# Kernel tuning notes

Measured on AMD Instinct MI355X. Metric: run time of the kernel, lower is better.

Reference implementation:

```python
import jax, jax.numpy as jnp
import numpy as np

N, T = 128, 20
E_IN, E_EMB, E_RNN = 2, 64, 256
N_IN, N_EMB, N_RNN, N_OUT = 2, 64, 128, 5
ATT = 64

# static edge index sets: diagonal = temporal edges (i,i), off-diagonal = spatial edges (i,j)
_DIAG = np.arange(N) * N + np.arange(N)
_OFFJ = np.array([[j for j in range(N) if j != i] for i in range(N)])  # [N, N-1]
_OFFD = (np.arange(N)[:, None] * N + _OFFJ).reshape(-1)               # [N*(N-1)]
_TEMP = (N - 1) / np.sqrt(ATT)  # attention temperature = num_edges / sqrt(attention_size)


def setup_inputs() -> dict:
    ks = iter(jax.random.split(jax.random.key(0), 40))
    def p(shape, s=0.05):
        return jax.random.normal(next(ks), shape, jnp.float32) * s
    return {
        "nodes": p((T, N, N_IN), 1.0),
        "edges": p((T, N * N, E_IN), 1.0),
        "h_edge0": jnp.zeros((N * N, E_RNN), jnp.float32),
        "c_edge0": jnp.zeros((N * N, E_RNN), jnp.float32),
        "h_node0": jnp.zeros((N, N_RNN), jnp.float32),
        "c_node0": jnp.zeros((N, N_RNN), jnp.float32),
        "t_enc_w": p((E_EMB, E_IN)), "t_enc_b": p((E_EMB,)),
        "t_wih": p((4 * E_RNN, E_EMB)), "t_whh": p((4 * E_RNN, E_RNN)),
        "t_bih": p((4 * E_RNN,)), "t_bhh": p((4 * E_RNN,)),
        "s_enc_w": p((E_EMB, E_IN)), "s_enc_b": p((E_EMB,)),
        "s_wih": p((4 * E_RNN, E_EMB)), "s_whh": p((4 * E_RNN, E_RNN)),
        "s_bih": p((4 * E_RNN,)), "s_bhh": p((4 * E_RNN,)),
        "att_t_w": p((ATT, E_RNN)), "att_t_b": p((ATT,)),
        "att_s_w": p((ATT, E_RNN)), "att_s_b": p((ATT,)),
        "n_enc_w": p((N_EMB, N_IN)), "n_enc_b": p((N_EMB,)),
        "n_attn_w": p((N_EMB, 2 * E_RNN)), "n_attn_b": p((N_EMB,)),
        "n_wih": p((4 * N_RNN, 2 * N_EMB)), "n_whh": p((4 * N_RNN, N_RNN)),
        "n_bih": p((4 * N_RNN,)), "n_bhh": p((4 * N_RNN,)),
        "out_w": p((N_OUT, N_RNN)), "out_b": p((N_OUT,)),
    }


def _lstm(x, h, c, wih, whh, bih, bhh):
    g = x @ wih.T + bih + h @ whh.T + bhh
    i, f, gg, o = jnp.split(g, 4, axis=-1)
    c2 = jax.nn.sigmoid(f) * c + jax.nn.sigmoid(i) * jnp.tanh(gg)
    return jax.nn.sigmoid(o) * jnp.tanh(c2), c2


def reference(nodes, edges, h_edge0, c_edge0, h_node0, c_node0,
              t_enc_w, t_enc_b, t_wih, t_whh, t_bih, t_bhh,
              s_enc_w, s_enc_b, s_wih, s_whh, s_bih, s_bhh,
              att_t_w, att_t_b, att_s_w, att_s_b,
              n_enc_w, n_enc_b, n_attn_w, n_attn_b,
              n_wih, n_whh, n_bih, n_bhh, out_w, out_b):
    def step(carry, xt):
        h_e, c_e, h_n, c_n = carry
        pos_t, edg_t = xt
        # temporal edge RNN on self edges (i,i)
        x_t = jax.nn.relu(edg_t[_DIAG] @ t_enc_w.T + t_enc_b)
        h_t, c_t = _lstm(x_t, h_e[_DIAG], c_e[_DIAG], t_wih, t_whh, t_bih, t_bhh)
        # spatial edge RNN on all pairwise edges (i,j), i != j
        x_s = jax.nn.relu(edg_t[_OFFD] @ s_enc_w.T + s_enc_b)
        h_s, c_s = _lstm(x_s, h_e[_OFFD], c_e[_OFFD], s_wih, s_whh, s_bih, s_bhh)
        h_e = h_e.at[_DIAG].set(h_t).at[_OFFD].set(h_s)
        c_e = c_e.at[_DIAG].set(c_t).at[_OFFD].set(c_s)
        # attention: each node attends over its N-1 spatial edge hidden states
        hs = h_s.reshape(N, N - 1, E_RNN)
        te = h_t @ att_t_w.T + att_t_b                          # [N, ATT]
        se = jnp.einsum('nkd,ad->nka', hs, att_s_w) + att_s_b   # [N, N-1, ATT]
        logits = jnp.einsum('nka,na->nk', se, te) * _TEMP
        w = jax.nn.softmax(logits, axis=-1)
        weighted = jnp.einsum('nk,nkd->nd', w, hs)              # [N, E_RNN]
        # node RNN
        enc = jax.nn.relu(pos_t @ n_enc_w.T + n_enc_b)
        h_edges = jnp.concatenate([h_t, weighted], axis=-1)
        h_emb = jax.nn.relu(h_edges @ n_attn_w.T + n_attn_b)
        h_n, c_n = _lstm(jnp.concatenate([enc, h_emb], axis=-1), h_n, c_n,
                         n_wih, n_whh, n_bih, n_bhh)
        out = h_n @ out_w.T + out_b
        return (h_e, c_e, h_n, c_n), out

    _, outs = jax.lax.scan(step, (h_edge0, c_edge0, h_node0, c_node0), (nodes, edges))
    return outs  # [T, N, 5]
```

## Files before the change

kernel.cpp:

```cpp
#include <hip/hip_runtime.h>
#include <cmath>

#define NN 128
#define TT 20
#define ERNN 256
#define TEMPSC 15.875f

typedef __attribute__((ext_vector_type(8))) short bf16x8;
typedef __attribute__((ext_vector_type(4))) float f32x4;

__device__ __forceinline__ float sigm(float x){ return 1.f/(1.f+__expf(-x)); }
__device__ __forceinline__ float ftanh(float x){ float e = __expf(2.f*x); return 1.f - 2.f/(e + 1.f); }
__device__ __forceinline__ float b2f(unsigned short u){ union{unsigned int i; float f;} v; v.i = ((unsigned int)u)<<16; return v.f; }
__device__ __forceinline__ unsigned short f2b(float x){ union{float f; unsigned int u;} v; v.f = x; unsigned int r = v.u + 0x7fffu + ((v.u>>16)&1u); return (unsigned short)(r>>16); }

typedef __attribute__((address_space(3))) unsigned int lds_u32;
typedef __attribute__((address_space(1))) unsigned int glb_u32;
__device__ __forceinline__ void glds16(const void* g, void* l){
    __builtin_amdgcn_global_load_lds((const glb_u32*)g, (lds_u32*)l, 16, 0, 0);
}

__device__ __forceinline__ size_t hoff(int r, int d){
    return ((size_t)((r>>7)*32 + (d>>3))*128 + (r&127))*8 + (d&7);
}

#define R_W2    (2*1024*320)
#define R_EB    2048
#define R_NWT   131072
#define R_NBS   512
#define R_HNN   16384
#define R_CNN   16384
#define R_INIT  (16384*32)
#define R_XENC  ((size_t)TT*16384*8)
#define PREP_TOT (R_W2 + R_EB + R_NWT + R_NBS + R_HNN + R_CNN + R_INIT + R_XENC)

__global__ void k_prep_all(
    const float* __restrict__ s_wih, const float* __restrict__ s_whh, unsigned short* __restrict__ s_wHi,
    const float* __restrict__ t_wih, const float* __restrict__ t_whh, unsigned short* __restrict__ t_wHi,
    const float* __restrict__ s_bih, const float* __restrict__ s_bhh, float* __restrict__ s_bs,
    const float* __restrict__ t_bih, const float* __restrict__ t_bhh, float* __restrict__ t_bs,
    const float* __restrict__ n_wih, const float* __restrict__ n_whh, float* __restrict__ n_wT,
    const float* __restrict__ n_bih, const float* __restrict__ n_bhh, float* __restrict__ n_bs,
    const float* __restrict__ h_n0, float* __restrict__ h_nn,
    const float* __restrict__ c_n0, float* __restrict__ c_nn,
    const float* __restrict__ h_e0, const float* __restrict__ c_e0,
    unsigned short* __restrict__ hHi, unsigned short* __restrict__ c_b,
    const float* __restrict__ edges,
    const float* __restrict__ s_enc_w, const float* __restrict__ s_enc_b,
    const float* __restrict__ t_enc_w, const float* __restrict__ t_enc_b,
    unsigned short* __restrict__ xe)
{
    size_t i = (size_t)blockIdx.x*256 + threadIdx.x;
    if (i < R_W2) {
        int idx = (int)i;
        int which = idx >= 1024*320;
        if (which) idx -= 1024*320;
        const float* wih = which ? t_wih : s_wih;
        const float* whh = which ? t_whh : s_whh;
        unsigned short* wHi = which ? t_wHi : s_wHi;
        int c = idx / 320, k = idx - c*320;
        int ch = ((c>>6)<<4) + (c&15), g = (c>>4)&3;
        int r = g*256 + ch;
        float v = (k < 64) ? wih[r*64 + k] : whh[r*256 + (k-64)];
        size_t dst = ((size_t)((c>>7)*40 + (k>>3))*128 + (c&127))*8 + (k&7);
        wHi[dst] = f2b(v);
        return;
    }
    i -= R_W2;
    if (i < R_EB) {
        int c = (int)i, which = c >= 1024;
        if (which) c -= 1024;
        const float* bih = which ? t_bih : s_bih;
        const float* bhh = which ? t_bhh : s_bhh;
        float* bs = which ? t_bs : s_bs;
        int ch = ((c>>6)<<4)+(c&15), g=(c>>4)&3;
        int r = g*256+ch;
        bs[c] = bih[r] + bhh[r];
        return;
    }
    i -= R_EB;
    if (i < R_NWT) {
        int j = (int)i;
        if (j < 65536) { int r = j >> 7, c = j & 127; n_wT[c*512 + r] = n_wih[j]; }
        else { j -= 65536; int r = j >> 7, c = j & 127; n_wT[(128 + c)*512 + r] = n_whh[j]; }
        return;
    }
    i -= R_NWT;
    if (i < R_NBS) { n_bs[i] = n_bih[i] + n_bhh[i]; return; }
    i -= R_NBS;
    if (i < R_HNN) { h_nn[i] = h_n0[i]; return; }
    i -= R_HNN;
    if (i < R_CNN) { c_nn[i] = c_n0[i]; return; }
    i -= R_CNN;
    if (i < R_INIT) {
        int g = (int)i;
        int d8 = g & 31, r = g >> 5;
        int row_ij;
        if (r < 16256){ int ii = r/127, jj = r - ii*127; row_ij = ii*NN + jj + (jj>=ii ? 1:0); }
        else          { row_ij = (r - 16256)*(NN+1); }
        const float* hs = h_e0 + (size_t)row_ij*ERNN + d8*8;
        const float* cs = c_e0 + (size_t)row_ij*ERNN + d8*8;
        bf16x8 hb, cb;
        #pragma unroll
        for (int q = 0; q < 8; ++q){ hb[q] = (short)f2b(hs[q]); cb[q] = (short)f2b(cs[q]); }
        *(bf16x8*)&hHi[hoff(r, d8*8)] = hb;
        *(bf16x8*)&c_b[(size_t)r*ERNN + d8*8] = cb;
        return;
    }
    i -= R_INIT;
    if (i < R_XENC) {
        size_t g = i;
        int row = (int)(g & 127);
        size_t rest = g >> 7;
        int kc = (int)(rest & 7);
        int tile = (int)((rest >> 3) & 127);
        int t = (int)(rest >> 10);
        int r = tile*128 + row;
        bool sp = (r < 16256);
        int row_ij;
        if (sp) { int ii = r/127, jj = r - ii*127; row_ij = ii*NN + jj + (jj>=ii ? 1:0); }
        else    { row_ij = (r - 16256)*(NN+1); }
        const float* w = sp ? s_enc_w : t_enc_w;
        const float* b = sp ? s_enc_b : t_enc_b;
        float e0 = edges[((size_t)t*16384 + row_ij)*2];
        float e1 = edges[((size_t)t*16384 + row_ij)*2 + 1];
        bf16x8 v8;
        #pragma unroll
        for (int q = 0; q < 8; ++q) {
            int m = kc*8 + q;
            v8[q] = (short)f2b(fmaxf(fmaf(w[m*2], e0, fmaf(w[m*2+1], e1, b[m])), 0.f));
        }
        *(bf16x8*)&xe[g*8] = v8;
    }
}

#define ESTEP(KS, NW) do { \
    asm volatile("s_waitcnt vmcnt(" #NW ")" ::: "memory"); \
    __builtin_amdgcn_s_barrier(); \
    __builtin_amdgcn_sched_barrier(0); \
    bf16x8 a0 = *(const bf16x8*)&Ah[(KS)&1][(kg*128 + arow)*8]; \
    bf16x8 a1 = *(const bf16x8*)&Ah[(KS)&1][(kg*128 + arow + 16)*8]; \
    bf16x8 b0 = *(const bf16x8*)&Bh[(KS)&1][(kg*128 + bcol)*8]; \
    bf16x8 b1 = *(const bf16x8*)&Bh[(KS)&1][(kg*128 + bcol + 16)*8]; \
    bf16x8 b2 = *(const bf16x8*)&Bh[(KS)&1][(kg*128 + bcol + 32)*8]; \
    bf16x8 b3 = *(const bf16x8*)&Bh[(KS)&1][(kg*128 + bcol + 48)*8]; \
    asm volatile("s_waitcnt lgkmcnt(0)" ::: "memory"); \
    __builtin_amdgcn_sched_barrier(0); \
    __builtin_amdgcn_s_barrier(); \
    if ((KS) + 2 <= 9) stage((KS)+2, (KS)&1); \
    acc[0][0] = __builtin_amdgcn_mfma_f32_16x16x32_bf16(a0, b0, acc[0][0],0,0,0); \
    acc[0][1] = __builtin_amdgcn_mfma_f32_16x16x32_bf16(a0, b1, acc[0][1],0,0,0); \
    acc[0][2] = __builtin_amdgcn_mfma_f32_16x16x32_bf16(a0, b2, acc[0][2],0,0,0); \
    acc[0][3] = __builtin_amdgcn_mfma_f32_16x16x32_bf16(a0, b3, acc[0][3],0,0,0); \
    acc[1][0] = __builtin_amdgcn_mfma_f32_16x16x32_bf16(a1, b0, acc[1][0],0,0,0); \
    acc[1][1] = __builtin_amdgcn_mfma_f32_16x16x32_bf16(a1, b1, acc[1][1],0,0,0); \
    acc[1][2] = __builtin_amdgcn_mfma_f32_16x16x32_bf16(a1, b2, acc[1][2],0,0,0); \
    acc[1][3] = __builtin_amdgcn_mfma_f32_16x16x32_bf16(a1, b3, acc[1][3],0,0,0); \
} while(0)

__global__ __launch_bounds__(512) void k_fused(
    const unsigned short* __restrict__ xenc_t,
    const unsigned short* __restrict__ h_in, unsigned short* __restrict__ h_out,
    unsigned short* __restrict__ hl_out, unsigned short* __restrict__ c_b,
    const unsigned short* __restrict__ s_wHi, const float* __restrict__ s_bs,
    const unsigned short* __restrict__ t_wHi, const float* __restrict__ t_bs,
    int has_node, int n_edge,
    const float* __restrict__ nodes_prev, const unsigned short* __restrict__ hl_prev,
    float* __restrict__ h_nn, float* __restrict__ c_nn, float* __restrict__ out_prev,
    const float* __restrict__ att_t_w, const float* __restrict__ att_t_b,
    const float* __restrict__ att_s_w, const float* __restrict__ att_s_b,
    const float* __restrict__ n_enc_w, const float* __restrict__ n_enc_b,
    const float* __restrict__ n_attn_w, const float* __restrict__ n_attn_b,
    const float* __restrict__ n_wT, const float* __restrict__ n_bsum,
    const float* __restrict__ out_w, const float* __restrict__ out_b)
{
    __shared__ __align__(16) char smem[32768];
    const int bid = blockIdx.x, tid = threadIdx.x;

    if (bid < NN) {
        if (!has_node) return;
        const int i = bid;
        float* sm  = (float*)smem;
        float* ht  = sm;
        float* te  = sm + 256;
        float* u   = sm + 320;
        float* lg  = sm + 576;
        float* cat = sm + 704;
        float* xc  = sm + 1216;
        float* hnl = sm + 1344;
        float* gl  = sm + 1472;
        float* pws = sm + 1984;
        float* msc = sm + 4032;

        if (tid < 256) ht[tid] = b2f(hl_prev[(size_t)(16256 + i)*256 + tid]);
        __syncthreads();
        if (tid < 256) {
            int m = tid >> 2, q = tid & 3;
            float s = 0.f;
            const float* wr = att_t_w + m*ERNN + q*64;
            const float* hh = ht + q*64;
            #pragma unroll 8
            for (int k = 0; k < 64; ++k) s = fmaf(wr[k], hh[k], s);
            s += __shfl_xor(s, 1);
            s += __shfl_xor(s, 2);
            if (q == 0) te[m] = s + att_t_b[m];
        }
        __syncthreads();
        if (tid < 256) {
            float s = 0.f;
            for (int m = 0; m < 64; ++m) s = fmaf(att_s_w[m*ERNN + tid], te[m], s);
            u[tid] = s;
        }
        if (tid == 320) {
            float s = 0.f;
            for (int m = 0; m < 64; ++m) s = fmaf(te[m], att_s_b[m], s);
            msc[2] = s;
        }
        __syncthreads();
        {
            int slot = tid >> 2, q = tid & 3;
            float part = 0.f;
            if (slot < 127) {
                const unsigned short* hs = hl_prev + (size_t)(i*127 + slot)*256 + q*64;
                const float* uu = u + q*64;
                #pragma unroll
                for (int d8 = 0; d8 < 8; ++d8) {
                    bf16x8 v = *(const bf16x8*)(hs + d8*8);
                    #pragma unroll
                    for (int j = 0; j < 8; ++j)
                        part = fmaf(uu[d8*8 + j], b2f((unsigned short)v[j]), part);
                }
            }
            part += __shfl_xor(part, 1);
            part += __shfl_xor(part, 2);
            if (slot < 127 && q == 0) lg[slot] = (part + msc[2]) * TEMPSC;
            if (tid == 511) lg[127] = -1e30f;
        }
        __syncthreads();
        if (tid < 64) {
            float a = fmaxf(lg[tid], lg[tid+64]);
            for (int off = 32; off; off >>= 1) a = fmaxf(a, __shfl_xor(a, off));
            if (tid == 0) msc[0] = a;
        }
        __syncthreads();
        if (tid < 128) lg[tid] = (tid < 127) ? __expf(lg[tid] - msc[0]) : 0.f;
        __syncthreads();
        if (tid < 64) {
            float a = lg[tid] + lg[tid+64];
            for (int off = 32; off; off >>= 1) a += __shfl_xor(a, off);
            if (tid == 0) msc[1] = a;
        }
        __syncthreads();
        {
            int w = tid >> 6, lane = tid & 63;
            float a0 = 0.f, a1 = 0.f, a2 = 0.f, a3 = 0.f;
            #pragma unroll 4
            for (int s = w*16; s < w*16 + 16; ++s) {
                int srow = (s < 127) ? s : 0;
                float wgt = lg[s];
                const unsigned short* hs = hl_prev + (size_t)(i*127 + srow)*256 + lane*4;
                ushort4 v = *(const ushort4*)hs;
                a0 = fmaf(wgt, b2f(v.x), a0);
                a1 = fmaf(wgt, b2f(v.y), a1);
                a2 = fmaf(wgt, b2f(v.z), a2);
                a3 = fmaf(wgt, b2f(v.w), a3);
            }
            pws[w*256 + lane*4+0] = a0; pws[w*256 + lane*4+1] = a1;
            pws[w*256 + lane*4+2] = a2; pws[w*256 + lane*4+3] = a3;
        }
        if (tid >= 256 && tid < 384) hnl[tid-256] = h_nn[i*128 + (tid-256)];
        __syncthreads();
        if (tid < 256) {
            float s = 0.f;
            #pragma unroll
            for (int w = 0; w < 8; ++w) s += pws[w*256 + tid];
            cat[256 + tid] = s / msc[1];
            cat[tid] = ht[tid];
        }
        __syncthreads();
        if (tid < 64) {
            float p0 = nodes_prev[i*2], p1 = nodes_prev[i*2+1];
            xc[tid] = fmaxf(fmaf(n_enc_w[tid*2], p0, fmaf(n_enc_w[tid*2+1], p1, n_enc_b[tid])), 0.f);
        }
        if (tid >= 256) {
            int t2 = tid - 256;
            int m = t2 >> 2, q = t2 & 3;
            float s = 0.f;
            const float* wr = n_attn_w + m*512 + q*128;
            const float* cc = cat + q*128;
            #pragma unroll 8
            for (int d = 0; d < 128; ++d) s = fmaf(wr[d], cc[d], s);
            s += __shfl_xor(s, 1);
            s += __shfl_xor(s, 2);
            if (q == 0) xc[64 + m] = fmaxf(s + n_attn_b[m], 0.f);
        }
        __syncthreads();
        {
            int n = tid;
            float s = n_bsum[n];
            for (int k = 0; k < 128; ++k) s = fmaf(n_wT[k*512 + n], xc[k], s);
            for (int k = 0; k < 128; ++k) s = fmaf(n_wT[(128+k)*512 + n], hnl[k], s);
            gl[n] = s;
        }
        __syncthreads();
        if (tid < 128) {
            float co = c_nn[i*128 + tid];
            float c2 = sigm(gl[128+tid])*co + sigm(gl[tid])*ftanh(gl[256+tid]);
            float h2 = sigm(gl[384+tid])*ftanh(c2);
            c_nn[i*128+tid] = c2;
            h_nn[i*128+tid] = h2;
            hnl[tid] = h2;
        }
        __syncthreads();
        if (tid < 5) {
            float s = out_b[tid];
            const float* wr = out_w + tid*128;
            for (int k = 0; k < 128; ++k) s = fmaf(wr[k], hnl[k], s);
            out_prev[i*5 + tid] = s;
        }
        return;
    }

    if (!n_edge) return;
    unsigned short (*Ah)[4096] = (unsigned short(*)[4096])smem;
    unsigned short (*Bh)[4096] = (unsigned short(*)[4096])(smem + 16384);
    const int ebid = bid - NN;
    const int lane = tid & 63, wid = tid >> 6;
    const int wg = (ebid & 7)*128 + (ebid >> 3);
    const int bm = wg >> 3, ntp = wg & 7;
    const bool sp = (bm < 127);
    const int rbase = bm * 128;
    const unsigned short* wHi = sp ? s_wHi : t_wHi;
    const float* bs = sp ? s_bs : t_bs;
    const int wr = wid & 3, wc = wid >> 2;
    const int nt = ntp*2 + wc;

    auto stage = [&](int ks, int b){
        int kc = wid >> 1, half = wid & 1;
        const unsigned short* asrc = (ks < 2)
            ? xenc_t + ((size_t)bm*8  + ks*4     + kc)*1024 + half*512
            : h_in   + ((size_t)bm*32 + (ks-2)*4 + kc)*1024 + half*512;
        glds16(asrc + lane*8, (char*)&Ah[b][0] + wid*1024);
        size_t wb = ((size_t)(ntp*40 + ks*4 + kc)*128 + half*64)*8;
        glds16(wHi + wb + lane*8, (char*)&Bh[b][0] + wid*1024);
    };
    stage(0, 0);
    stage(1, 1);

    f32x4 acc[2][4];
    #pragma unroll
    for (int m = 0; m < 2; ++m)
        #pragma unroll
        for (int g = 0; g < 4; ++g)
            acc[m][g] = (f32x4){0.f,0.f,0.f,0.f};

    const int arow = wr*32 + (lane & 15);
    const int bcol = wc*64 + (lane & 15);
    const int kg = lane >> 4;

    ESTEP(0, 2);
    ESTEP(1, 2);
    ESTEP(2, 2);
    ESTEP(3, 2);
    ESTEP(4, 2);
    ESTEP(5, 2);
    ESTEP(6, 2);
    ESTEP(7, 2);
    ESTEP(8, 2);
    ESTEP(9, 0);

    const int chl = lane & 15, q4 = (lane >> 4)*4;
    const int ch = nt*16 + chl;
    const int cbase = nt*64 + chl;
    const float b0 = bs[cbase], b1 = bs[cbase+16], b2 = bs[cbase+32], b3 = bs[cbase+48];
    #pragma unroll
    for (int m = 0; m < 2; ++m) {
        #pragma unroll
        for (int rg = 0; rg < 4; ++rg) {
            int lrow = wr*32 + m*16 + q4 + rg;
            int row = rbase + lrow;
            float gi = acc[m][0][rg] + b0;
            float gf = acc[m][1][rg] + b1;
            float gg = acc[m][2][rg] + b2;
            float go = acc[m][3][rg] + b3;
            size_t off = (size_t)row*256 + ch;
            float c_old = b2f(c_b[off]);
            float c2 = sigm(gf)*c_old + sigm(gi)*ftanh(gg);
            float h2 = sigm(go)*ftanh(c2);
            c_b[off] = f2b(c2);
            unsigned short hb = f2b(h2);
            h_out[((size_t)(bm*32 + (ch>>3))*128 + lrow)*8 + (ch&7)] = hb;
            hl_out[off] = hb;
        }
    }
}

extern "C" void kernel_launch(void* const* d_in, const int* in_sizes, int n_in,
                              void* d_out, int out_size, void* d_ws, size_t ws_size,
                              hipStream_t stream)
{
    const float* nodes   = (const float*)d_in[0];
    const float* edges   = (const float*)d_in[1];
    const float* h_e0    = (const float*)d_in[2];
    const float* c_e0    = (const float*)d_in[3];
    const float* h_n0    = (const float*)d_in[4];
    const float* c_n0    = (const float*)d_in[5];
    const float* t_enc_w = (const float*)d_in[6];
    const float* t_enc_b = (const float*)d_in[7];
    const float* t_wih   = (const float*)d_in[8];
    const float* t_whh   = (const float*)d_in[9];
    const float* t_bih   = (const float*)d_in[10];
    const float* t_bhh   = (const float*)d_in[11];
    const float* s_enc_w = (const float*)d_in[12];
    const float* s_enc_b = (const float*)d_in[13];
    const float* s_wih   = (const float*)d_in[14];
    const float* s_whh   = (const float*)d_in[15];
    const float* s_bih   = (const float*)d_in[16];
    const float* s_bhh   = (const float*)d_in[17];
    const float* att_t_w = (const float*)d_in[18];
    const float* att_t_b = (const float*)d_in[19];
    const float* att_s_w = (const float*)d_in[20];
    const float* att_s_b = (const float*)d_in[21];
    const float* n_enc_w = (const float*)d_in[22];
    const float* n_enc_b = (const float*)d_in[23];
    const float* n_attn_w= (const float*)d_in[24];
    const float* n_attn_b= (const float*)d_in[25];
    const float* n_wih   = (const float*)d_in[26];
    const float* n_whh   = (const float*)d_in[27];
    const float* n_bih   = (const float*)d_in[28];
    const float* n_bhh   = (const float*)d_in[29];
    const float* out_w   = (const float*)d_in[30];
    const float* out_b   = (const float*)d_in[31];
    float* out = (float*)d_out;

    char* p = (char*)d_ws;
    float* h_nn  = (float*)p;            p += 128*128*4;
    float* c_nn  = (float*)p;            p += 128*128*4;
    float* s_bs  = (float*)p;            p += 1024*4;
    float* t_bs  = (float*)p;            p += 1024*4;
    float* n_wT  = (float*)p;            p += 256*512*4;
    float* n_bs  = (float*)p;            p += 512*4;
    unsigned short* c_b  = (unsigned short*)p;  p += (size_t)16384*256*2;
    unsigned short* h_a  = (unsigned short*)p;  p += (size_t)16384*256*2;
    unsigned short* h_b  = (unsigned short*)p;  p += (size_t)16384*256*2;
    unsigned short* hl_a = (unsigned short*)p;  p += (size_t)16384*256*2;
    unsigned short* hl_b = (unsigned short*)p;  p += (size_t)16384*256*2;
    unsigned short* xenc = (unsigned short*)p;  p += (size_t)TT*16384*64*2;
    unsigned short* s_wHi = (unsigned short*)p; p += 1024*320*2;
    unsigned short* t_wHi = (unsigned short*)p; p += 1024*320*2;

    int prep_blocks = (int)((PREP_TOT + 255) / 256);
    k_prep_all<<<prep_blocks, 256, 0, stream>>>(
        s_wih, s_whh, s_wHi, t_wih, t_whh, t_wHi,
        s_bih, s_bhh, s_bs, t_bih, t_bhh, t_bs,
        n_wih, n_whh, n_wT, n_bih, n_bhh, n_bs,
        h_n0, h_nn, c_n0, c_nn,
        h_e0, c_e0, h_a, c_b,
        edges, s_enc_w, s_enc_b, t_enc_w, t_enc_b, xenc);

    for (int t = 0; t < TT; ++t) {
        const unsigned short* h_in  = (t & 1) ? h_b : h_a;
        unsigned short*       h_out = (t & 1) ? h_a : h_b;
        unsigned short*       hl_out= (t & 1) ? hl_b : hl_a;
        const unsigned short* hl_prev=(t & 1) ? hl_a : hl_b;
        const float* nprev = (t > 0) ? nodes + (size_t)(t-1)*NN*2 : nodes;
        float* oprev = (t > 0) ? out + (size_t)(t-1)*NN*5 : out;
        k_fused<<<NN + 1024, 512, 0, stream>>>(xenc + (size_t)t*16384*64,
            h_in, h_out, hl_out, c_b,
            s_wHi, s_bs, t_wHi, t_bs,
            (t > 0) ? 1 : 0, 1024,
            nprev, hl_prev, h_nn, c_nn, oprev,
            att_t_w, att_t_b, att_s_w, att_s_b, n_enc_w, n_enc_b,
            n_attn_w, n_attn_b, n_wT, n_bs, out_w, out_b);
    }
    k_fused<<<NN, 512, 0, stream>>>(xenc,
        h_a, h_b, hl_a, c_b,
        s_wHi, s_bs, t_wHi, t_bs,
        1, 0,
        nodes + (size_t)19*NN*2, hl_b, h_nn, c_nn, out + (size_t)19*NN*5,
        att_t_w, att_t_b, att_s_w, att_s_b, n_enc_w, n_enc_b,
        n_attn_w, n_attn_b, n_wT, n_bs, out_w, out_b);
}
```

Measured before the change: 609.5 us.

## Shrink fused kernel blocks to 256 threads, single-buffer MFMA tiles, fp32 attention hidden states

Drops the fused step kernel from 512 to 256 threads per block and doubles the edge-GEMM grid, so each block computes a 128x64 tile instead of 128x128. The double-buffered, hand-scheduled MFMA pipeline becomes a simple single-buffered loop with syncthreads. Shared memory shrinks, which should allow more resident blocks. The node/attention path now reads fp32 edge hidden states instead of bf16 and uses simpler per-thread loops with fewer parallel partial reductions. The trade is losing load/compute overlap in the GEMM and doubling the bytes written and read for the attention copy of h.

```diff
diff --git a/kernel.cpp b/kernel.cpp
--- a/kernel.cpp
+++ b/kernel.cpp
@@ -134,38 +134,14 @@
     }
 }
 
-#define ESTEP(KS, NW) do { \
-    asm volatile("s_waitcnt vmcnt(" #NW ")" ::: "memory"); \
-    __builtin_amdgcn_s_barrier(); \
-    __builtin_amdgcn_sched_barrier(0); \
-    bf16x8 a0 = *(const bf16x8*)&Ah[(KS)&1][(kg*128 + arow)*8]; \
-    bf16x8 a1 = *(const bf16x8*)&Ah[(KS)&1][(kg*128 + arow + 16)*8]; \
-    bf16x8 b0 = *(const bf16x8*)&Bh[(KS)&1][(kg*128 + bcol)*8]; \
-    bf16x8 b1 = *(const bf16x8*)&Bh[(KS)&1][(kg*128 + bcol + 16)*8]; \
-    bf16x8 b2 = *(const bf16x8*)&Bh[(KS)&1][(kg*128 + bcol + 32)*8]; \
-    bf16x8 b3 = *(const bf16x8*)&Bh[(KS)&1][(kg*128 + bcol + 48)*8]; \
-    asm volatile("s_waitcnt lgkmcnt(0)" ::: "memory"); \
-    __builtin_amdgcn_sched_barrier(0); \
-    __builtin_amdgcn_s_barrier(); \
-    if ((KS) + 2 <= 9) stage((KS)+2, (KS)&1); \
-    acc[0][0] = __builtin_amdgcn_mfma_f32_16x16x32_bf16(a0, b0, acc[0][0],0,0,0); \
-    acc[0][1] = __builtin_amdgcn_mfma_f32_16x16x32_bf16(a0, b1, acc[0][1],0,0,0); \
-    acc[0][2] = __builtin_amdgcn_mfma_f32_16x16x32_bf16(a0, b2, acc[0][2],0,0,0); \
-    acc[0][3] = __builtin_amdgcn_mfma_f32_16x16x32_bf16(a0, b3, acc[0][3],0,0,0); \
-    acc[1][0] = __builtin_amdgcn_mfma_f32_16x16x32_bf16(a1, b0, acc[1][0],0,0,0); \
-    acc[1][1] = __builtin_amdgcn_mfma_f32_16x16x32_bf16(a1, b1, acc[1][1],0,0,0); \
-    acc[1][2] = __builtin_amdgcn_mfma_f32_16x16x32_bf16(a1, b2, acc[1][2],0,0,0); \
-    acc[1][3] = __builtin_amdgcn_mfma_f32_16x16x32_bf16(a1, b3, acc[1][3],0,0,0); \
-} while(0)
-
-__global__ __launch_bounds__(512) void k_fused(
+__global__ __launch_bounds__(256, 8) void k_fused(
     const unsigned short* __restrict__ xenc_t,
     const unsigned short* __restrict__ h_in, unsigned short* __restrict__ h_out,
-    unsigned short* __restrict__ hl_out, unsigned short* __restrict__ c_b,
+    float* __restrict__ hf_out, unsigned short* __restrict__ c_b,
     const unsigned short* __restrict__ s_wHi, const float* __restrict__ s_bs,
     const unsigned short* __restrict__ t_wHi, const float* __restrict__ t_bs,
     int has_node, int n_edge,
-    const float* __restrict__ nodes_prev, const unsigned short* __restrict__ hl_prev,
+    const float* __restrict__ nodes_prev, const float* __restrict__ hf_prev,
     float* __restrict__ h_nn, float* __restrict__ c_nn, float* __restrict__ out_prev,
     const float* __restrict__ att_t_w, const float* __restrict__ att_t_b,
     const float* __restrict__ att_s_w, const float* __restrict__ att_s_b,
@@ -174,7 +150,7 @@
     const float* __restrict__ n_wT, const float* __restrict__ n_bsum,
     const float* __restrict__ out_w, const float* __restrict__ out_b)
 {
-    __shared__ __align__(16) char smem[32768];
+    __shared__ __align__(16) char smem[12544];
     const int bid = blockIdx.x, tid = threadIdx.x;
 
     if (bid < NN) {
@@ -189,52 +165,45 @@
         float* xc  = sm + 1216;
         float* hnl = sm + 1344;
         float* gl  = sm + 1472;
-        float* pws = sm + 1984;
-        float* msc = sm + 4032;
-
-        if (tid < 256) ht[tid] = b2f(hl_prev[(size_t)(16256 + i)*256 + tid]);
-        __syncthreads();
-        if (tid < 256) {
-            int m = tid >> 2, q = tid & 3;
-            float s = 0.f;
-            const float* wr = att_t_w + m*ERNN + q*64;
-            const float* hh = ht + q*64;
-            #pragma unroll 8
-            for (int k = 0; k < 64; ++k) s = fmaf(wr[k], hh[k], s);
-            s += __shfl_xor(s, 1);
-            s += __shfl_xor(s, 2);
-            if (q == 0) te[m] = s + att_t_b[m];
-        }
-        __syncthreads();
-        if (tid < 256) {
+        float* msc = sm + 1984;
+        const float* h = hf_prev;
+
+        ht[tid] = h[(size_t)(16256 + i)*256 + tid];
+        __syncthreads();
+        if (tid < 64) {
+            float s = att_t_b[tid];
+            const float* wr = att_t_w + tid*ERNN;
+            for (int k = 0; k < ERNN; ++k) s = fmaf(wr[k], ht[k], s);
+            te[tid] = s;
+        }
+        __syncthreads();
+        {
             float s = 0.f;
             for (int m = 0; m < 64; ++m) s = fmaf(att_s_w[m*ERNN + tid], te[m], s);
             u[tid] = s;
         }
-        if (tid == 320) {
+        if (tid == 0) {
             float s = 0.f;
             for (int m = 0; m < 64; ++m) s = fmaf(te[m], att_s_b[m], s);
             msc[2] = s;
         }
         __syncthreads();
         {
-            int slot = tid >> 2, q = tid & 3;
+            int slot = tid >> 1, half = tid & 1;
             float part = 0.f;
             if (slot < 127) {
-                const unsigned short* hs = hl_prev + (size_t)(i*127 + slot)*256 + q*64;
-                const float* uu = u + q*64;
-                #pragma unroll
-                for (int d8 = 0; d8 < 8; ++d8) {
-                    bf16x8 v = *(const bf16x8*)(hs + d8*8);
-                    #pragma unroll
-                    for (int j = 0; j < 8; ++j)
-                        part = fmaf(uu[d8*8 + j], b2f((unsigned short)v[j]), part);
+                const float4* hs = (const float4*)(h + (size_t)(i*127 + slot)*256 + half*128);
+                const float4* uu = (const float4*)(u + half*128);
+                #pragma unroll 8
+                for (int d = 0; d < 32; ++d) {
+                    float4 a = hs[d], b = uu[d];
+                    part = fmaf(a.x, b.x, part); part = fmaf(a.y, b.y, part);
+                    part = fmaf(a.z, b.z, part); part = fmaf(a.w, b.w, part);
                 }
             }
             part += __shfl_xor(part, 1);
-            part += __shfl_xor(part, 2);
-            if (slot < 127 && q == 0) lg[slot] = (part + msc[2]) * TEMPSC;
-            if (tid == 511) lg[127] = -1e30f;
+            if (slot < 127 && (half == 0)) lg[slot] = (part + msc[2]) * TEMPSC;
+            if (tid == 255) lg[127] = -1e30f;
         }
         __syncthreads();
         if (tid < 64) {
@@ -244,6 +213,7 @@
         }
         __syncthreads();
         if (tid < 128) lg[tid] = (tid < 127) ? __expf(lg[tid] - msc[0]) : 0.f;
+        else hnl[tid-128] = h_nn[i*128 + (tid-128)];
         __syncthreads();
         if (tid < 64) {
             float a = lg[tid] + lg[tid+64];
@@ -252,51 +222,27 @@
         }
         __syncthreads();
         {
-            int w = tid >> 6, lane = tid & 63;
-            float a0 = 0.f, a1 = 0.f, a2 = 0.f, a3 = 0.f;
-            #pragma unroll 4
-            for (int s = w*16; s < w*16 + 16; ++s) {
-                int srow = (s < 127) ? s : 0;
-                float wgt = lg[s];
-                const unsigned short* hs = hl_prev + (size_t)(i*127 + srow)*256 + lane*4;
-                ushort4 v = *(const ushort4*)hs;
-                a0 = fmaf(wgt, b2f(v.x), a0);
-                a1 = fmaf(wgt, b2f(v.y), a1);
-                a2 = fmaf(wgt, b2f(v.z), a2);
-                a3 = fmaf(wgt, b2f(v.w), a3);
-            }
-            pws[w*256 + lane*4+0] = a0; pws[w*256 + lane*4+1] = a1;
-            pws[w*256 + lane*4+2] = a2; pws[w*256 + lane*4+3] = a3;
-        }
-        if (tid >= 256 && tid < 384) hnl[tid-256] = h_nn[i*128 + (tid-256)];
-        __syncthreads();
-        if (tid < 256) {
-            float s = 0.f;
-            #pragma unroll
-            for (int w = 0; w < 8; ++w) s += pws[w*256 + tid];
-            cat[256 + tid] = s / msc[1];
+            float acc = 0.f;
+            for (int slot = 0; slot < 127; ++slot)
+                acc = fmaf(lg[slot], h[(size_t)(i*127 + slot)*256 + tid], acc);
             cat[tid] = ht[tid];
+            cat[256 + tid] = acc / msc[1];
         }
         __syncthreads();
         if (tid < 64) {
             float p0 = nodes_prev[i*2], p1 = nodes_prev[i*2+1];
             xc[tid] = fmaxf(fmaf(n_enc_w[tid*2], p0, fmaf(n_enc_w[tid*2+1], p1, n_enc_b[tid])), 0.f);
-        }
-        if (tid >= 256) {
-            int t2 = tid - 256;
-            int m = t2 >> 2, q = t2 & 3;
-            float s = 0.f;
-            const float* wr = n_attn_w + m*512 + q*128;
-            const float* cc = cat + q*128;
-            #pragma unroll 8
-            for (int d = 0; d < 128; ++d) s = fmaf(wr[d], cc[d], s);
-            s += __shfl_xor(s, 1);
-            s += __shfl_xor(s, 2);
-            if (q == 0) xc[64 + m] = fmaxf(s + n_attn_b[m], 0.f);
-        }
-        __syncthreads();
-        {
-            int n = tid;
+        } else if (tid < 128) {
+            int m = tid - 64;
+            float s = n_attn_b[m];
+            const float* wr = n_attn_w + m*512;
+            for (int d = 0; d < 512; ++d) s = fmaf(wr[d], cat[d], s);
+            xc[tid] = fmaxf(s, 0.f);
+        }
+        __syncthreads();
+        #pragma unroll
+        for (int rep = 0; rep < 2; ++rep) {
+            int n = tid + rep*256;
             float s = n_bsum[n];
             for (int k = 0; k < 128; ++k) s = fmaf(n_wT[k*512 + n], xc[k], s);
             for (int k = 0; k < 128; ++k) s = fmaf(n_wT[(128+k)*512 + n], hnl[k], s);
@@ -322,30 +268,28 @@
     }
 
     if (!n_edge) return;
-    unsigned short (*Ah)[4096] = (unsigned short(*)[4096])smem;
-    unsigned short (*Bh)[4096] = (unsigned short(*)[4096])(smem + 16384);
+    unsigned short* Ah = (unsigned short*)smem;
+    unsigned short* Bh = (unsigned short*)(smem + 8192);
     const int ebid = bid - NN;
     const int lane = tid & 63, wid = tid >> 6;
-    const int wg = (ebid & 7)*128 + (ebid >> 3);
-    const int bm = wg >> 3, ntp = wg & 7;
+    const int wg = (ebid & 7)*256 + (ebid >> 3);
+    const int bm = wg >> 4, nt = wg & 15;
     const bool sp = (bm < 127);
     const int rbase = bm * 128;
     const unsigned short* wHi = sp ? s_wHi : t_wHi;
     const float* bs = sp ? s_bs : t_bs;
-    const int wr = wid & 3, wc = wid >> 2;
-    const int nt = ntp*2 + wc;
-
-    auto stage = [&](int ks, int b){
-        int kc = wid >> 1, half = wid & 1;
+    const int nt128 = nt >> 1, colh = (nt & 1)*64;
+
+    auto stage = [&](int ks){
         const unsigned short* asrc = (ks < 2)
-            ? xenc_t + ((size_t)bm*8  + ks*4     + kc)*1024 + half*512
-            : h_in   + ((size_t)bm*32 + (ks-2)*4 + kc)*1024 + half*512;
-        glds16(asrc + lane*8, (char*)&Ah[b][0] + wid*1024);
-        size_t wb = ((size_t)(ntp*40 + ks*4 + kc)*128 + half*64)*8;
-        glds16(wHi + wb + lane*8, (char*)&Bh[b][0] + wid*1024);
+            ? xenc_t + ((size_t)bm*8  + ks*4     + wid)*1024
+            : h_in   + ((size_t)bm*32 + (ks-2)*4 + wid)*1024;
+        glds16(asrc + lane*8,       (char*)Ah + wid*2048);
+        glds16(asrc + 512 + lane*8, (char*)Ah + wid*2048 + 1024);
+        size_t wb = ((size_t)(nt128*40 + ks*4 + wid)*128 + colh)*8 + lane*8;
+        glds16(wHi + wb, (char*)Bh + wid*1024);
     };
-    stage(0, 0);
-    stage(1, 1);
+    stage(0);
 
     f32x4 acc[2][4];
     #pragma unroll
@@ -354,20 +298,25 @@
         for (int g = 0; g < 4; ++g)
             acc[m][g] = (f32x4){0.f,0.f,0.f,0.f};
 
-    const int arow = wr*32 + (lane & 15);
-    const int bcol = wc*64 + (lane & 15);
+    const int arow = wid*32 + (lane & 15);
+    const int bcol = lane & 15;
     const int kg = lane >> 4;
-
-    ESTEP(0, 2);
-    ESTEP(1, 2);
-    ESTEP(2, 2);
-    ESTEP(3, 2);
-    ESTEP(4, 2);
-    ESTEP(5, 2);
-    ESTEP(6, 2);
-    ESTEP(7, 2);
-    ESTEP(8, 2);
-    ESTEP(9, 0);
+    for (int ks = 0; ; ++ks) {
+        __syncthreads();
+        bf16x8 a[2], bb[4];
+        #pragma unroll
+        for (int m = 0; m < 2; ++m) a[m] = *(const bf16x8*)&Ah[(kg*128 + arow + m*16)*8];
+        #pragma unroll
+        for (int g = 0; g < 4; ++g) bb[g] = *(const bf16x8*)&Bh[(kg*64 + bcol + g*16)*8];
+        #pragma unroll
+        for (int m = 0; m < 2; ++m)
+            #pragma unroll
+            for (int g = 0; g < 4; ++g)
+                acc[m][g] = __builtin_amdgcn_mfma_f32_16x16x32_bf16(a[m], bb[g], acc[m][g], 0, 0, 0);
+        if (ks == 9) break;
+        __syncthreads();
+        stage(ks+1);
+    }
 
     const int chl = lane & 15, q4 = (lane >> 4)*4;
     const int ch = nt*16 + chl;
@@ -377,7 +326,7 @@
     for (int m = 0; m < 2; ++m) {
         #pragma unroll
         for (int rg = 0; rg < 4; ++rg) {
-            int lrow = wr*32 + m*16 + q4 + rg;
+            int lrow = wid*32 + m*16 + q4 + rg;
             int row = rbase + lrow;
             float gi = acc[m][0][rg] + b0;
             float gf = acc[m][1][rg] + b1;
@@ -388,9 +337,8 @@
             float c2 = sigm(gf)*c_old + sigm(gi)*ftanh(gg);
             float h2 = sigm(go)*ftanh(c2);
             c_b[off] = f2b(c2);
-            unsigned short hb = f2b(h2);
-            h_out[((size_t)(bm*32 + (ch>>3))*128 + lrow)*8 + (ch&7)] = hb;
-            hl_out[off] = hb;
+            h_out[((size_t)(bm*32 + (ch>>3))*128 + lrow)*8 + (ch&7)] = f2b(h2);
+            hf_out[off] = h2;
         }
     }
 }
@@ -440,11 +388,11 @@
     float* t_bs  = (float*)p;            p += 1024*4;
     float* n_wT  = (float*)p;            p += 256*512*4;
     float* n_bs  = (float*)p;            p += 512*4;
+    float* hf_a  = (float*)p;            p += (size_t)16384*256*4;
+    float* hf_b  = (float*)p;            p += (size_t)16384*256*4;
     unsigned short* c_b  = (unsigned short*)p;  p += (size_t)16384*256*2;
     unsigned short* h_a  = (unsigned short*)p;  p += (size_t)16384*256*2;
     unsigned short* h_b  = (unsigned short*)p;  p += (size_t)16384*256*2;
-    unsigned short* hl_a = (unsigned short*)p;  p += (size_t)16384*256*2;
-    unsigned short* hl_b = (unsigned short*)p;  p += (size_t)16384*256*2;
     unsigned short* xenc = (unsigned short*)p;  p += (size_t)TT*16384*64*2;
     unsigned short* s_wHi = (unsigned short*)p; p += 1024*320*2;
     unsigned short* t_wHi = (unsigned short*)p; p += 1024*320*2;
@@ -461,23 +409,23 @@
     for (int t = 0; t < TT; ++t) {
         const unsigned short* h_in  = (t & 1) ? h_b : h_a;
         unsigned short*       h_out = (t & 1) ? h_a : h_b;
-        unsigned short*       hl_out= (t & 1) ? hl_b : hl_a;
-        const unsigned short* hl_prev=(t & 1) ? hl_a : hl_b;
+        float*       hf_out = (t & 1) ? hf_b : hf_a;
+        const float* hf_prev= (t & 1) ? hf_a : hf_b;
         const float* nprev = (t > 0) ? nodes + (size_t)(t-1)*NN*2 : nodes;
         float* oprev = (t > 0) ? out + (size_t)(t-1)*NN*5 : out;
-        k_fused<<<NN + 1024, 512, 0, stream>>>(xenc + (size_t)t*16384*64,
-            h_in, h_out, hl_out, c_b,
+        k_fused<<<NN + 2048, 256, 0, stream>>>(xenc + (size_t)t*16384*64,
+            h_in, h_out, hf_out, c_b,
             s_wHi, s_bs, t_wHi, t_bs,
-            (t > 0) ? 1 : 0, 1024,
-            nprev, hl_prev, h_nn, c_nn, oprev,
+            (t > 0) ? 1 : 0, 1,
+            nprev, hf_prev, h_nn, c_nn, oprev,
             att_t_w, att_t_b, att_s_w, att_s_b, n_enc_w, n_enc_b,
             n_attn_w, n_attn_b, n_wT, n_bs, out_w, out_b);
     }
-    k_fused<<<NN, 512, 0, stream>>>(xenc,
-        h_a, h_b, hl_a, c_b,
+    k_fused<<<NN, 256, 0, stream>>>(xenc,
+        h_a, h_b, hf_a, c_b,
         s_wHi, s_bs, t_wHi, t_bs,
         1, 0,
-        nodes + (size_t)19*NN*2, hl_b, h_nn, c_nn, out + (size_t)19*NN*5,
+        nodes + (size_t)19*NN*2, hf_b, h_nn, c_nn, out + (size_t)19*NN*5,
         att_t_w, att_t_b, att_s_w, att_s_b, n_enc_w, n_enc_b,
         n_attn_w, n_attn_b, n_wT, n_bs, out_w, out_b);
 }
```

Measured after the change: 1.226 ms. +101.2%, slower.
